# Kernel tuning notes

Measured on AMD Instinct MI355X. Metric: run time of the kernel, lower is better.

## Reference

```python
import jax, jax.numpy as jnp
import numpy as np

TAU = 2.0
V_TH = 1.0
V_RESET = 0.0
ATAN_ALPHA = 2.0  # spikingjelly surrogate.ATan default


def setup_inputs() -> dict:
    key = jax.random.key(0)
    k1, k2 = jax.random.split(key)
    B, T, N = 64, 200, 4096
    x = jax.random.normal(k1, (B, T, N), dtype=jnp.float32)
    # nn.Parameter(torch.ones(1, size) * v_threshold) -- unused in math but part of module
    threshold = jnp.ones((1, N), dtype=jnp.float32) * V_TH
    return {"x": x, "threshold": threshold}


def _lif_scan(x):
    # x: [B, T, N] -> spikes: [B, T, N]
    xt = jnp.swapaxes(x, 0, 1)  # [T, B, N]
    v0 = jnp.full(xt.shape[1:], V_RESET, dtype=x.dtype)

    def step(v, x_t):
        # decay_input=True: v += (x - (v - v_reset)) / tau
        v = v + (x_t - (v - V_RESET)) / TAU
        s = (v - V_TH >= 0).astype(v.dtype)
        # hard reset
        v = v * (1.0 - s) + V_RESET * s
        return v, s

    _, spikes = jax.lax.scan(step, v0, xt)
    return jnp.swapaxes(spikes, 0, 1)  # [B, T, N]


def reference(x, threshold):
    # threshold param is expanded but never used in the original forward
    return _lif_scan(x)
```

## Files before the change

kernel.cpp:

```cpp
#include <hip/hip_runtime.h>


constexpr int B = 64;
constexpr int T = 200;
constexpr int N = 4096;
constexpr int N4 = N / 4;

__global__ __launch_bounds__(256) void lif_kernel(const float4* __restrict__ x,
                                                  float4* __restrict__ out) {
    const int idx = blockIdx.x * blockDim.x + threadIdx.x;
    const int b = idx >> 10;
    const int n = idx & (N4 - 1);

    const float4* __restrict__ xp = x + (size_t)b * (T * N4) + n;
    float4* __restrict__ op = out + (size_t)b * (T * N4) + n;

    float4 v = {0.0f, 0.0f, 0.0f, 0.0f};

#pragma unroll 8
    for (int t = 0; t < T; ++t) {
        const float4 xv = xp[t * N4];
        float4 s;
        v.x = v.x + (xv.x - v.x) * 0.5f;
        v.y = v.y + (xv.y - v.y) * 0.5f;
        v.z = v.z + (xv.z - v.z) * 0.5f;
        v.w = v.w + (xv.w - v.w) * 0.5f;

        s.x = (v.x >= 1.0f) ? 1.0f : 0.0f;
        s.y = (v.y >= 1.0f) ? 1.0f : 0.0f;
        s.z = (v.z >= 1.0f) ? 1.0f : 0.0f;
        s.w = (v.w >= 1.0f) ? 1.0f : 0.0f;

        v.x = (v.x >= 1.0f) ? 0.0f : v.x;
        v.y = (v.y >= 1.0f) ? 0.0f : v.y;
        v.z = (v.z >= 1.0f) ? 0.0f : v.z;
        v.w = (v.w >= 1.0f) ? 0.0f : v.w;

        op[t * N4] = s;
    }
}

extern "C" void kernel_launch(void* const* d_in, const int* in_sizes, int n_in,
                              void* d_out, int out_size, void* d_ws, size_t ws_size,
                              hipStream_t stream) {
    const float4* x = (const float4*)d_in[0];
    float4* out = (float4*)d_out;

    const int threads = B * N4;
    const int block = 256;
    const int grid = threads / block;
    lif_kernel<<<grid, block, 0, stream>>>(x, out);
}
```

Measured before the change: 337.3 us.

## Halve vector width, add register prefetch pipeline and nontemporal memory ops

Switches each thread from float4 to float2 columns, doubling the number of threads along the parallel batch/neuron dimension. Adds an 8-deep register ring buffer that issues loads several timesteps ahead of use, and uses nontemporal loads and stores for the streaming data. The aim is more memory-level parallelism in this latency-bound sequential scan. In exchange each access is narrower and register use goes up.

```diff
diff --git a/kernel.cpp b/kernel.cpp
--- a/kernel.cpp
+++ b/kernel.cpp
@@ -1,52 +1,61 @@
 #include <hip/hip_runtime.h>
 
+
+typedef float vfloat2 __attribute__((ext_vector_type(2)));
 
 constexpr int B = 64;
 constexpr int T = 200;
 constexpr int N = 4096;
-constexpr int N4 = N / 4;
+constexpr int N2 = N / 2;
+constexpr int PF = 8;
 
-__global__ __launch_bounds__(256) void lif_kernel(const float4* __restrict__ x,
-                                                  float4* __restrict__ out) {
+__global__ __launch_bounds__(256) void lif_kernel(const vfloat2* __restrict__ x,
+                                                  vfloat2* __restrict__ out) {
     const int idx = blockIdx.x * blockDim.x + threadIdx.x;
-    const int b = idx >> 10;
-    const int n = idx & (N4 - 1);
+    const int b = idx >> 11;
+    const int n = idx & (N2 - 1);
 
-    const float4* __restrict__ xp = x + (size_t)b * (T * N4) + n;
-    float4* __restrict__ op = out + (size_t)b * (T * N4) + n;
+    const vfloat2* __restrict__ xp = x + (size_t)b * (T * N2) + n;
+    vfloat2* __restrict__ op = out + (size_t)b * (T * N2) + n;
 
-    float4 v = {0.0f, 0.0f, 0.0f, 0.0f};
+    vfloat2 buf[PF];
+#pragma unroll
+    for (int j = 0; j < PF; ++j) {
+        buf[j] = __builtin_nontemporal_load(&xp[j * N2]);
+    }
 
-#pragma unroll 8
-    for (int t = 0; t < T; ++t) {
-        const float4 xv = xp[t * N4];
-        float4 s;
-        v.x = v.x + (xv.x - v.x) * 0.5f;
-        v.y = v.y + (xv.y - v.y) * 0.5f;
-        v.z = v.z + (xv.z - v.z) * 0.5f;
-        v.w = v.w + (xv.w - v.w) * 0.5f;
+    vfloat2 v = {0.0f, 0.0f};
 
-        s.x = (v.x >= 1.0f) ? 1.0f : 0.0f;
-        s.y = (v.y >= 1.0f) ? 1.0f : 0.0f;
-        s.z = (v.z >= 1.0f) ? 1.0f : 0.0f;
-        s.w = (v.w >= 1.0f) ? 1.0f : 0.0f;
+    for (int t = 0; t < T; t += PF) {
+#pragma unroll
+        for (int j = 0; j < PF; ++j) {
+            const vfloat2 xv = buf[j];
+            const int tn = t + j + PF;
+            if (tn < T) {
+                buf[j] = __builtin_nontemporal_load(&xp[tn * N2]);
+            }
 
-        v.x = (v.x >= 1.0f) ? 0.0f : v.x;
-        v.y = (v.y >= 1.0f) ? 0.0f : v.y;
-        v.z = (v.z >= 1.0f) ? 0.0f : v.z;
-        v.w = (v.w >= 1.0f) ? 0.0f : v.w;
+            v.x = v.x + (xv.x - v.x) * 0.5f;
+            v.y = v.y + (xv.y - v.y) * 0.5f;
 
-        op[t * N4] = s;
+            vfloat2 s;
+            s.x = (v.x >= 1.0f) ? 1.0f : 0.0f;
+            s.y = (v.y >= 1.0f) ? 1.0f : 0.0f;
+            v.x = (v.x >= 1.0f) ? 0.0f : v.x;
+            v.y = (v.y >= 1.0f) ? 0.0f : v.y;
+
+            __builtin_nontemporal_store(s, &op[(t + j) * N2]);
+        }
     }
 }
 
 extern "C" void kernel_launch(void* const* d_in, const int* in_sizes, int n_in,
                               void* d_out, int out_size, void* d_ws, size_t ws_size,
                               hipStream_t stream) {
-    const float4* x = (const float4*)d_in[0];
-    float4* out = (float4*)d_out;
+    const vfloat2* x = (const vfloat2*)d_in[0];
+    vfloat2* out = (vfloat2*)d_out;
 
-    const int threads = B * N4;
+    const int threads = B * N2;
     const int block = 256;
     const int grid = threads / block;
     lif_kernel<<<grid, block, 0, stream>>>(x, out);
```

After: 406.0 us. 20.4% more time.

## Software-pipeline loads in groups of eight and use nontemporal stores

Applied to the files above, without the earlier changes.

Restructures the time loop into groups of 8 steps: it prefetches the next group's 8 inputs into registers while the current group is computed, then finishes with an epilogue group. Output spikes are written with nontemporal stores so the write stream does not pollute the cache. The aim is more memory-level parallelism per thread in this bandwidth-bound scan, paid for with extra registers that could lower occupancy.

```diff
diff --git a/kernel.cpp b/kernel.cpp
--- a/kernel.cpp
+++ b/kernel.cpp
@@ -1,50 +1,91 @@
 #include <hip/hip_runtime.h>
 
+
+typedef float vfloat4 __attribute__((ext_vector_type(4)));
 
 constexpr int B = 64;
 constexpr int T = 200;
 constexpr int N = 4096;
 constexpr int N4 = N / 4;
+constexpr int G = 8;
+constexpr int NG = T / G;
 
-__global__ __launch_bounds__(256) void lif_kernel(const float4* __restrict__ x,
-                                                  float4* __restrict__ out) {
+__global__ __launch_bounds__(256) void lif_kernel(const vfloat4* __restrict__ x,
+                                                  vfloat4* __restrict__ out) {
     const int idx = blockIdx.x * blockDim.x + threadIdx.x;
     const int b = idx >> 10;
     const int n = idx & (N4 - 1);
 
-    const float4* __restrict__ xp = x + (size_t)b * (T * N4) + n;
-    float4* __restrict__ op = out + (size_t)b * (T * N4) + n;
+    const vfloat4* __restrict__ xp = x + (size_t)b * (T * N4) + n;
+    vfloat4* __restrict__ op = out + (size_t)b * (T * N4) + n;
 
-    float4 v = {0.0f, 0.0f, 0.0f, 0.0f};
+    vfloat4 buf[G], nbuf[G];
+#pragma unroll
+    for (int j = 0; j < G; ++j) buf[j] = xp[j * N4];
 
-#pragma unroll 8
-    for (int t = 0; t < T; ++t) {
-        const float4 xv = xp[t * N4];
-        float4 s;
-        v.x = v.x + (xv.x - v.x) * 0.5f;
-        v.y = v.y + (xv.y - v.y) * 0.5f;
-        v.z = v.z + (xv.z - v.z) * 0.5f;
-        v.w = v.w + (xv.w - v.w) * 0.5f;
+    vfloat4 v = {0.0f, 0.0f, 0.0f, 0.0f};
 
-        s.x = (v.x >= 1.0f) ? 1.0f : 0.0f;
-        s.y = (v.y >= 1.0f) ? 1.0f : 0.0f;
-        s.z = (v.z >= 1.0f) ? 1.0f : 0.0f;
-        s.w = (v.w >= 1.0f) ? 1.0f : 0.0f;
+    for (int g = 0; g < NG - 1; ++g) {
+        const int base = g * G;
 
-        v.x = (v.x >= 1.0f) ? 0.0f : v.x;
-        v.y = (v.y >= 1.0f) ? 0.0f : v.y;
-        v.z = (v.z >= 1.0f) ? 0.0f : v.z;
-        v.w = (v.w >= 1.0f) ? 0.0f : v.w;
+#pragma unroll
+        for (int j = 0; j < G; ++j) nbuf[j] = xp[(base + G + j) * N4];
 
-        op[t * N4] = s;
+#pragma unroll
+        for (int j = 0; j < G; ++j) {
+            const vfloat4 xv = buf[j];
+            v.x = v.x + (xv.x - v.x) * 0.5f;
+            v.y = v.y + (xv.y - v.y) * 0.5f;
+            v.z = v.z + (xv.z - v.z) * 0.5f;
+            v.w = v.w + (xv.w - v.w) * 0.5f;
+
+            vfloat4 s;
+            s.x = (v.x >= 1.0f) ? 1.0f : 0.0f;
+            s.y = (v.y >= 1.0f) ? 1.0f : 0.0f;
+            s.z = (v.z >= 1.0f) ? 1.0f : 0.0f;
+            s.w = (v.w >= 1.0f) ? 1.0f : 0.0f;
+            v.x = (v.x >= 1.0f) ? 0.0f : v.x;
+            v.y = (v.y >= 1.0f) ? 0.0f : v.y;
+            v.z = (v.z >= 1.0f) ? 0.0f : v.z;
+            v.w = (v.w >= 1.0f) ? 0.0f : v.w;
+
+            __builtin_nontemporal_store(s, &op[(base + j) * N4]);
+        }
+
+#pragma unroll
+        for (int j = 0; j < G; ++j) buf[j] = nbuf[j];
+    }
+
+    {
+        const int base = (NG - 1) * G;
+#pragma unroll
+        for (int j = 0; j < G; ++j) {
+            const vfloat4 xv = buf[j];
+            v.x = v.x + (xv.x - v.x) * 0.5f;
+            v.y = v.y + (xv.y - v.y) * 0.5f;
+            v.z = v.z + (xv.z - v.z) * 0.5f;
+            v.w = v.w + (xv.w - v.w) * 0.5f;
+
+            vfloat4 s;
+            s.x = (v.x >= 1.0f) ? 1.0f : 0.0f;
+            s.y = (v.y >= 1.0f) ? 1.0f : 0.0f;
+            s.z = (v.z >= 1.0f) ? 1.0f : 0.0f;
+            s.w = (v.w >= 1.0f) ? 1.0f : 0.0f;
+            v.x = (v.x >= 1.0f) ? 0.0f : v.x;
+            v.y = (v.y >= 1.0f) ? 0.0f : v.y;
+            v.z = (v.z >= 1.0f) ? 0.0f : v.z;
+            v.w = (v.w >= 1.0f) ? 0.0f : v.w;
+
+            __builtin_nontemporal_store(s, &op[(base + j) * N4]);
+        }
     }
 }
 
 extern "C" void kernel_launch(void* const* d_in, const int* in_sizes, int n_in,
                               void* d_out, int out_size, void* d_ws, size_t ws_size,
                               hipStream_t stream) {
-    const float4* x = (const float4*)d_in[0];
-    float4* out = (float4*)d_out;
+    const vfloat4* x = (const vfloat4*)d_in[0];
+    vfloat4* out = (vfloat4*)d_out;
 
     const int threads = B * N4;
     const int block = 256;
```

Result: slower. 344.2 us (+2.1%).
